# Kernel optimization log

Measured on AMD Instinct MI355X. Metric: run time of the kernel, lower is better.

Reference implementation:

```python
import jax, jax.numpy as jnp
import numpy as np

NMUL = 16
NASH = 3
NEARZERO = 1e-5
TIMESTEP_D = 1.0
LENF = 15

PARAM_BOUNDS = [
    ("schaake_const", 0.0, 0.1), ("smcmax", 0.3, 0.6), ("soil_depth", 0.5, 3.0),
    ("wltsmc", 0.05, 0.2), ("satpsi", 0.01, 0.5), ("bb", 2.0, 12.0),
    ("mult", 100.0, 2000.0), ("satdk", 1e-7, 1e-4), ("slop", 0.0, 1.0),
    ("max_gw_storage", 0.01, 0.5), ("Cgw", 1e-6, 1e-3), ("expon", 1.0, 8.0),
    ("K_nash", 0.01, 0.5),
]
ROUT_BOUNDS = [("rout_a", 0.0, 2.9), ("rout_b", 0.0, 6.5)]


def setup_inputs() -> dict:
    key = jax.random.key(0)
    k1, k2 = jax.random.split(key)
    T, B = 730, 2048
    # prcp ~ U[0,20) mm/d, pet ~ U[0,8) mm/d
    x_phy = jax.random.uniform(k1, (T, B, 2), dtype=jnp.float32) * jnp.array([20.0, 8.0], jnp.float32)
    n_static = len(PARAM_BOUNDS) * NMUL + len(ROUT_BOUNDS)  # 210
    phy_static = jax.random.uniform(k2, (B, n_static), dtype=jnp.float32)
    return {"x_phy": x_phy, "phy_static": phy_static}


def _cfe_forward(x_phy, phy_static):
    T, B, _ = x_phy.shape
    n_phys = len(PARAM_BOUNDS)
    # descale: change_param_range(p, [lb, ub]) = p * (ub - lb) + lb
    phys = phy_static[:, : n_phys * NMUL].reshape(B, n_phys, NMUL)
    prm = {name: phys[:, i, :] * (ub - lb) + lb for i, (name, lb, ub) in enumerate(PARAM_BOUNDS)}
    route_raw = phy_static[:, n_phys * NMUL :]
    rout = {name: route_raw[:, i] * (ub - lb) + lb for i, (name, lb, ub) in enumerate(ROUT_BOUNDS)}

    P = jnp.repeat(x_phy[:, :, 0:1], NMUL, axis=2)    # [T,B,NMUL]
    PET = jnp.repeat(x_phy[:, :, 1:2], NMUL, axis=2)  # [T,B,NMUL]

    soil0 = jnp.full((B, NMUL), 0.05, jnp.float32)
    gw0 = jnp.full((B, NMUL), 0.01, jnp.float32)
    nash0 = jnp.full((B, NMUL, NASH), NEARZERO, jnp.float32)

    max_soil = prm["smcmax"] * prm["soil_depth"]
    # Clapp-Hornberger field-capacity threshold from satpsi, bb
    fc_frac = jnp.clip((prm["satpsi"] / prm["soil_depth"]) ** (1.0 / prm["bb"]), 0.0, 1.0)
    fc_threshold = prm["smcmax"] * fc_frac * prm["soil_depth"]

    def step(carry, forc):
        soil, gw, nash = carry
        p, pet = forc
        # --- ET: first from rainfall, then Budyko-type from soil ---
        et_rain = jnp.minimum(p, pet)
        p_rem = p - et_rain
        pet_rem = pet - et_rain
        smc = soil / prm["soil_depth"]
        budyko = jnp.clip((smc - prm["wltsmc"]) / (prm["smcmax"] - prm["wltsmc"] + NEARZERO), 0.0, 1.0)
        aet_soil = jnp.minimum(pet_rem * budyko, jnp.maximum(soil - NEARZERO, 0.0))
        soil = soil - aet_soil
        aet = et_rain + aet_soil
        # --- Schaake infiltration / runoff partitioning ---
        deficit = jnp.maximum(max_soil - soil, 0.0)
        infil_cap = deficit * (1.0 - jnp.exp(-prm["schaake_const"] * TIMESTEP_D))
        runoff = p_rem * p_rem / (p_rem + infil_cap + NEARZERO)
        runoff = jnp.minimum(runoff, p_rem)
        infiltration = jnp.minimum(p_rem - runoff, deficit)
        runoff = p_rem - infiltration
        soil = soil + infiltration
        # --- soil dual-outlet nonlinear reservoir (percolation + lateral) ---
        above = jnp.maximum(soil - fc_threshold, 0.0)
        frac = above / jnp.maximum(max_soil - fc_threshold, NEARZERO)
        perc = prm["satdk"] * prm["mult"] * TIMESTEP_D * frac
        lat = prm["satdk"] * prm["mult"] * prm["slop"] * TIMESTEP_D * frac
        tot = perc + lat
        scale = jnp.minimum(1.0, above / jnp.maximum(tot, NEARZERO))
        perc = perc * scale
        lat = lat * scale
        soil = soil - perc - lat
        # --- groundwater exponential reservoir ---
        gw = gw + perc
        q_gw = prm["Cgw"] * jnp.expm1(prm["expon"] * jnp.clip(gw / prm["max_gw_storage"], 0.0, 1.0))
        q_gw = jnp.clip(q_gw, 0.0, jnp.maximum(gw - NEARZERO, 0.0))
        gw = gw - q_gw
        # --- Nash cascade routing of lateral flow (3 linear reservoirs) ---
        inflow = lat
        K = prm["K_nash"]
        new_nash = []
        for i in range(NASH):
            s = nash[..., i] + inflow
            out = K * s
            new_nash.append(s - out)
            inflow = out
        nash = jnp.stack(new_nash, axis=-1)
        q_lat = inflow
        q_sim = runoff + q_lat + q_gw
        return (soil, gw, nash), (q_sim, runoff, q_lat, q_gw, aet, soil, gw)

    _, outs = jax.lax.scan(step, (soil0, gw0, nash0), (P, PET))
    q_sim = outs[0]                 # [T,B,NMUL]
    q_avg = q_sim.mean(-1)          # [T,B]  multi-model averaging

    # --- gamma unit-hydrograph routing (uh_gamma + causal uh_conv) ---
    a = jax.nn.relu(rout["rout_a"])[:, None] + 0.1    # [B,1]
    th = jax.nn.relu(rout["rout_b"])[:, None] + 0.5   # [B,1]
    t = (jnp.arange(LENF, dtype=jnp.float32) + 0.5)[None, :]  # [1,LENF]
    w = t ** (a - 1.0) * jnp.exp(-t / th) / (jnp.exp(jax.lax.lgamma(a)) * th ** a)
    w = w / w.sum(1, keepdims=True)                    # [B,LENF]
    xp = jnp.pad(q_avg, ((LENF - 1, 0), (0, 0)))       # causal pad on time axis
    stream = sum(
        w[None, :, j] * jax.lax.dynamic_slice_in_dim(xp, LENF - 1 - j, T, 0)
        for j in range(LENF)
    )
    return stream[..., None]  # [T,B,1] routed streamflow


def reference(x_phy, phy_static):
    return _cfe_forward(x_phy, phy_static)
```

## Files before the change

### kernel.cpp

```cpp
#include <hip/hip_runtime.h>
#include <math.h>


constexpr int T_STEPS = 730;
constexpr int BATCH   = 2048;
constexpr int NMULC   = 16;
constexpr int LENFC   = 15;
constexpr int NPHYS   = 13;
constexpr int NSTAT   = NPHYS * NMULC + 2;
constexpr float NZ    = 1e-5f;
constexpr float INV_NZ= 1e5f;
constexpr int NCH     = 2;
constexpr int LPB     = 8;
constexpr int TB      = 15;
constexpr int T_MAIN  = 720;

__device__ __forceinline__ float frcp(float x) { return __builtin_amdgcn_rcpf(x); }

__device__ __forceinline__ float dpp_sum8(float x) {
    int v;
    v = __builtin_amdgcn_update_dpp(0, __float_as_int(x), 0xB1, 0xF, 0xF, true);
    x += __int_as_float(v);
    v = __builtin_amdgcn_update_dpp(0, __float_as_int(x), 0x4E, 0xF, 0xF, true);
    x += __int_as_float(v);
    v = __builtin_amdgcn_update_dpp(0, __float_as_int(x), 0x141, 0xF, 0xF, true);
    x += __int_as_float(v);
    return x;
}

struct Prm {
    float k1[NCH], k2[NCH], ms[NCH], fc[NCH], ic[NCH], cc[NCH], pc[NCH],
          lc[NCH], sc[NCH], e2[NCH], Km[NCH], Kk[NCH], Cg[NCH], ig[NCH];
    float w[LENFC];
};
struct St { float soil[NCH], gw[NCH], n0[NCH], n1[NCH], n2[NCH]; };

template <int SLOT>
__device__ __forceinline__ float substep(const Prm& P, St& S,
                                         float (&ring)[LENFC], const float2 fv)
{
    const float p = fv.x, pet = fv.y;
    const float et      = fminf(p, pet);
    const float p_rem   = p - et;
    const float pet_rem = pet - et;
    const float prem_nz = p_rem + NZ;
    const float prem_sq = p_rem * p_rem;

    float qsum = 0.0f;
    #pragma unroll
    for (int c = 0; c < NCH; ++c) {
        float budyko = fmaf(S.soil[c], P.k1[c], P.k2[c]);
        budyko = fminf(fmaxf(budyko, 0.0f), 1.0f);
        const float aet = fminf(pet_rem * budyko, S.soil[c] - NZ);
        float so = S.soil[c] - aet;

        const float deficit = P.ms[c] - so;
        const float den     = fmaf(deficit, P.ic[c], prem_nz);
        const float runoff0 = prem_sq * frcp(den);
        const float infil   = fminf(p_rem - runoff0, deficit);
        const float runoff  = p_rem - infil;
        so += infil;

        const float above = fmaxf(so - P.fc[c], 0.0f);
        const float asc   = fminf(above * P.sc[c], above * above * INV_NZ);
        const float lat   = P.lc[c] * asc;
        so = fmaf(-P.cc[c], asc, so);
        S.soil[c] = so;

        float g = fmaf(P.pc[c], asc, S.gw[c]);
        const float ratio = fminf(g * P.ig[c], 1.0f);
        const float qg0   = fmaf(P.Cg[c], __builtin_amdgcn_exp2f(P.e2[c] * ratio), -P.Cg[c]);
        const float qg    = fminf(qg0, g - NZ);
        S.gw[c] = g - qg;

        const float s0 = S.n0[c] + lat;             const float s1 = fmaf(P.Kk[c], s0, S.n1[c]);
        const float s2 = fmaf(P.Kk[c], s1, S.n2[c]); const float o2 = P.Kk[c] * s2;
        S.n0[c] = P.Km[c] * s0; S.n1[c] = P.Km[c] * s1; S.n2[c] = P.Km[c] * s2;

        qsum += runoff + o2 + qg;
    }

    ring[SLOT] = qsum;
    float c0 = 0.0f, c1 = 0.0f, c2 = 0.0f, c3 = 0.0f;
    #pragma unroll
    for (int j = 0; j < LENFC; j += 4) {
        c0 = fmaf(P.w[j], ring[(SLOT - j + 15) % 15], c0);
        if (j + 1 < LENFC) c1 = fmaf(P.w[j + 1], ring[(SLOT - j - 1 + 30) % 15], c1);
        if (j + 2 < LENFC) c2 = fmaf(P.w[j + 2], ring[(SLOT - j - 2 + 30) % 15], c2);
        if (j + 3 < LENFC) c3 = fmaf(P.w[j + 3], ring[(SLOT - j - 3 + 30) % 15], c3);
    }
    return (c0 + c1) + (c2 + c3);
}

#define SUBST(s) { const float acc = substep<(s)>(P, S, ring, f[(s)]);           \
                   const float r = dpp_sum8(acc);                                \
                   if (lane0) out[(tb + (s)) * BATCH + b] = r; }
#define DO15(X) X(0) X(1) X(2) X(3) X(4) X(5) X(6) X(7) X(8) X(9) X(10) X(11) X(12) X(13) X(14)
#define DO10(X) X(0) X(1) X(2) X(3) X(4) X(5) X(6) X(7) X(8) X(9)

__global__ __launch_bounds__(64, 1)
void cfe_kernel(const float* __restrict__ x,
                const float* __restrict__ ps,
                float* __restrict__ out)
{
    const int tid = blockIdx.x * 64 + threadIdx.x;
    const int b   = tid >> 3;
    const int m0  = tid & 7;
    const bool lane0 = (m0 == 0);

    const float* __restrict__ row = ps + b * NSTAT;

    Prm P;
    #pragma unroll
    for (int c = 0; c < NCH; ++c) {
        const int m = m0 + c * 8;
        const float schaake    = row[ 0*NMULC + m] * 0.1f;
        const float smcmax     = row[ 1*NMULC + m] * 0.3f   + 0.3f;
        const float soil_depth = row[ 2*NMULC + m] * 2.5f   + 0.5f;
        const float wltsmc     = row[ 3*NMULC + m] * 0.15f  + 0.05f;
        const float satpsi     = row[ 4*NMULC + m] * 0.49f  + 0.01f;
        const float bb_        = row[ 5*NMULC + m] * 10.0f  + 2.0f;
        const float multp      = row[ 6*NMULC + m] * 1900.0f+ 100.0f;
        const float satdk      = row[ 7*NMULC + m] * (1e-4f - 1e-7f) + 1e-7f;
        const float slop       = row[ 8*NMULC + m];
        const float max_gw     = row[ 9*NMULC + m] * 0.49f  + 0.01f;
        P.Cg[c]                = row[10*NMULC + m] * (1e-3f - 1e-6f) + 1e-6f;
        const float expon      = row[11*NMULC + m] * 7.0f   + 1.0f;
        P.Kk[c]                = row[12*NMULC + m] * 0.49f  + 0.01f;

        const float inv_sd  = 1.0f / soil_depth;
        const float bud_den = 1.0f / (smcmax - wltsmc + NZ);
        P.k1[c] = inv_sd * bud_den;
        P.k2[c] = -wltsmc * bud_den;
        P.ms[c] = smcmax * soil_depth;
        float fc_frac = powf(satpsi * inv_sd, 1.0f / bb_);
        fc_frac = fminf(fmaxf(fc_frac, 0.0f), 1.0f);
        P.fc[c] = smcmax * fc_frac * soil_depth;
        P.ic[c] = 1.0f - expf(-schaake);
        const float sm  = satdk * multp;
        const float sml = sm * slop;
        const float inv_mft = 1.0f / fmaxf(P.ms[c] - P.fc[c], NZ);
        P.ig[c] = 1.0f / max_gw;
        P.cc[c] = inv_mft * (sm + sml);
        P.pc[c] = sm  * inv_mft;
        P.lc[c] = sml * inv_mft;
        P.sc[c] = fminf(1.0f, 1.0f / P.cc[c]);
        P.e2[c] = expon * 1.442695041f;
        P.Km[c] = 1.0f - P.Kk[c];
    }

    {
        const float rout_a = row[NPHYS*NMULC + 0] * 2.9f;
        const float rout_b = row[NPHYS*NMULC + 1] * 6.5f;
        const float a  = fmaxf(rout_a, 0.0f) + 0.1f;
        const float th = fmaxf(rout_b, 0.0f) + 0.5f;
        float wsum = 0.0f;
        #pragma unroll
        for (int j = 0; j < LENFC; ++j) {
            const float tj = (float)j + 0.5f;
            P.w[j] = powf(tj, a - 1.0f) * expf(-tj / th);
            wsum += P.w[j];
        }
        const float wscale = 1.0f / (wsum * (float)NMULC);
        #pragma unroll
        for (int j = 0; j < LENFC; ++j) P.w[j] *= wscale;
    }

    St S;
    #pragma unroll
    for (int c = 0; c < NCH; ++c) {
        S.soil[c] = 0.05f; S.gw[c] = 0.01f;
        S.n0[c] = NZ; S.n1[c] = NZ; S.n2[c] = NZ;
    }
    float ring[LENFC];
    #pragma unroll
    for (int j = 0; j < LENFC; ++j) ring[j] = 0.0f;

    const float2* __restrict__ xp = (const float2*)x;

    #pragma unroll 1
    for (int tb = 0; tb < T_MAIN; tb += TB) {
        float2 f[TB];
        #pragma unroll
        for (int s = 0; s < TB; ++s) f[s] = xp[(tb + s) * BATCH + b];
        DO15(SUBST)
    }

    {
        const int tb = T_MAIN;
        float2 f[10];
        #pragma unroll
        for (int s = 0; s < 10; ++s) f[s] = xp[(tb + s) * BATCH + b];
        DO10(SUBST)
    }
}

extern "C" void kernel_launch(void* const* d_in, const int* in_sizes, int n_in,
                              void* d_out, int out_size, void* d_ws, size_t ws_size,
                              hipStream_t stream) {
    const float* x_phy      = (const float*)d_in[0];
    const float* phy_static = (const float*)d_in[1];
    float* out = (float*)d_out;

    const int total = BATCH * LPB;
    const int block = 64;
    const int grid  = total / block;
    cfe_kernel<<<grid, block, 0, stream>>>(x_phy, phy_static, out);
}
```

Measured before the change: 177.4 us.

## Double-buffer forcing loads and vectorize per-lane physics with float2 ops

Result: faster. 156.0 us (-12.1%).

```diff
diff --git a/kernel.cpp b/kernel.cpp
--- a/kernel.cpp
+++ b/kernel.cpp
@@ -15,7 +15,12 @@
 constexpr int TB      = 15;
 constexpr int T_MAIN  = 720;
 
+typedef float v2f __attribute__((ext_vector_type(2)));
+
 __device__ __forceinline__ float frcp(float x) { return __builtin_amdgcn_rcpf(x); }
+__device__ __forceinline__ v2f v2(float s) { return (v2f){s, s}; }
+__device__ __forceinline__ v2f vmin(v2f a, v2f b) { return __builtin_elementwise_min(a, b); }
+__device__ __forceinline__ v2f vmax(v2f a, v2f b) { return __builtin_elementwise_max(a, b); }
 
 __device__ __forceinline__ float dpp_sum8(float x) {
     int v;
@@ -29,11 +34,10 @@
 }
 
 struct Prm {
-    float k1[NCH], k2[NCH], ms[NCH], fc[NCH], ic[NCH], cc[NCH], pc[NCH],
-          lc[NCH], sc[NCH], e2[NCH], Km[NCH], Kk[NCH], Cg[NCH], ig[NCH];
+    v2f k1, k2, ms, fc, ic, cc, pc, lc, sc, e2, Km, Kk, Cg, ig;
     float w[LENFC];
 };
-struct St { float soil[NCH], gw[NCH], n0[NCH], n1[NCH], n2[NCH]; };
+struct St { v2f soil, gw, n0, n1, n2; };
 
 template <int SLOT>
 __device__ __forceinline__ float substep(const Prm& P, St& S,
@@ -46,39 +50,42 @@
     const float prem_nz = p_rem + NZ;
     const float prem_sq = p_rem * p_rem;
 
-    float qsum = 0.0f;
-    #pragma unroll
-    for (int c = 0; c < NCH; ++c) {
-        float budyko = fmaf(S.soil[c], P.k1[c], P.k2[c]);
-        budyko = fminf(fmaxf(budyko, 0.0f), 1.0f);
-        const float aet = fminf(pet_rem * budyko, S.soil[c] - NZ);
-        float so = S.soil[c] - aet;
-
-        const float deficit = P.ms[c] - so;
-        const float den     = fmaf(deficit, P.ic[c], prem_nz);
-        const float runoff0 = prem_sq * frcp(den);
-        const float infil   = fminf(p_rem - runoff0, deficit);
-        const float runoff  = p_rem - infil;
-        so += infil;
-
-        const float above = fmaxf(so - P.fc[c], 0.0f);
-        const float asc   = fminf(above * P.sc[c], above * above * INV_NZ);
-        const float lat   = P.lc[c] * asc;
-        so = fmaf(-P.cc[c], asc, so);
-        S.soil[c] = so;
-
-        float g = fmaf(P.pc[c], asc, S.gw[c]);
-        const float ratio = fminf(g * P.ig[c], 1.0f);
-        const float qg0   = fmaf(P.Cg[c], __builtin_amdgcn_exp2f(P.e2[c] * ratio), -P.Cg[c]);
-        const float qg    = fminf(qg0, g - NZ);
-        S.gw[c] = g - qg;
-
-        const float s0 = S.n0[c] + lat;             const float s1 = fmaf(P.Kk[c], s0, S.n1[c]);
-        const float s2 = fmaf(P.Kk[c], s1, S.n2[c]); const float o2 = P.Kk[c] * s2;
-        S.n0[c] = P.Km[c] * s0; S.n1[c] = P.Km[c] * s1; S.n2[c] = P.Km[c] * s2;
-
-        qsum += runoff + o2 + qg;
-    }
+    v2f budyko = S.soil * P.k1 + P.k2;
+    budyko = vmin(vmax(budyko, v2(0.0f)), v2(1.0f));
+    const v2f aet = vmin(v2(pet_rem) * budyko, S.soil - v2(NZ));
+    v2f so = S.soil - aet;
+
+    const v2f deficit = P.ms - so;
+    const v2f den     = deficit * P.ic + v2(prem_nz);
+    v2f rden; rden.x = frcp(den.x); rden.y = frcp(den.y);
+    const v2f runoff0 = v2(prem_sq) * rden;
+    const v2f infil   = vmin(v2(p_rem) - runoff0, deficit);
+    const v2f runoff  = v2(p_rem) - infil;
+    so += infil;
+
+    const v2f above = vmax(so - P.fc, v2(0.0f));
+    const v2f asc   = vmin(above * P.sc, above * above * v2(INV_NZ));
+    const v2f lat   = P.lc * asc;
+    so = so - P.cc * asc;
+    S.soil = so;
+
+    v2f g = P.pc * asc + S.gw;
+    const v2f ratio = vmin(g * P.ig, v2(1.0f));
+    v2f ex;
+    ex.x = __builtin_amdgcn_exp2f(P.e2.x * ratio.x);
+    ex.y = __builtin_amdgcn_exp2f(P.e2.y * ratio.y);
+    const v2f qg0 = P.Cg * ex - P.Cg;
+    const v2f qg  = vmin(qg0, g - v2(NZ));
+    S.gw = g - qg;
+
+    const v2f s0 = S.n0 + lat;
+    const v2f s1 = P.Kk * s0 + S.n1;
+    const v2f s2 = P.Kk * s1 + S.n2;
+    const v2f o2 = P.Kk * s2;
+    S.n0 = P.Km * s0; S.n1 = P.Km * s1; S.n2 = P.Km * s2;
+
+    const v2f qv = runoff + o2 + qg;
+    const float qsum = qv.x + qv.y;
 
     ring[SLOT] = qsum;
     float c0 = 0.0f, c1 = 0.0f, c2 = 0.0f, c3 = 0.0f;
@@ -92,11 +99,21 @@
     return (c0 + c1) + (c2 + c3);
 }
 
-#define SUBST(s) { const float acc = substep<(s)>(P, S, ring, f[(s)]);           \
-                   const float r = dpp_sum8(acc);                                \
-                   if (lane0) out[(tb + (s)) * BATCH + b] = r; }
-#define DO15(X) X(0) X(1) X(2) X(3) X(4) X(5) X(6) X(7) X(8) X(9) X(10) X(11) X(12) X(13) X(14)
-#define DO10(X) X(0) X(1) X(2) X(3) X(4) X(5) X(6) X(7) X(8) X(9)
+#define SUBST(s, FBUF, TBASE) {                                              \
+    const float acc = substep<(s)>(P, S, ring, FBUF[(s)]);                   \
+    const float r = dpp_sum8(acc);                                           \
+    if (lane0) out[((TBASE) + (s)) * BATCH + b] = r; }
+#define DO15(FBUF, TBASE) \
+    SUBST(0,FBUF,TBASE) SUBST(1,FBUF,TBASE) SUBST(2,FBUF,TBASE)  \
+    SUBST(3,FBUF,TBASE) SUBST(4,FBUF,TBASE) SUBST(5,FBUF,TBASE)  \
+    SUBST(6,FBUF,TBASE) SUBST(7,FBUF,TBASE) SUBST(8,FBUF,TBASE)  \
+    SUBST(9,FBUF,TBASE) SUBST(10,FBUF,TBASE) SUBST(11,FBUF,TBASE)\
+    SUBST(12,FBUF,TBASE) SUBST(13,FBUF,TBASE) SUBST(14,FBUF,TBASE)
+#define DO10(FBUF, TBASE) \
+    SUBST(0,FBUF,TBASE) SUBST(1,FBUF,TBASE) SUBST(2,FBUF,TBASE)  \
+    SUBST(3,FBUF,TBASE) SUBST(4,FBUF,TBASE) SUBST(5,FBUF,TBASE)  \
+    SUBST(6,FBUF,TBASE) SUBST(7,FBUF,TBASE) SUBST(8,FBUF,TBASE)  \
+    SUBST(9,FBUF,TBASE)
 
 __global__ __launch_bounds__(64, 1)
 void cfe_kernel(const float* __restrict__ x,
@@ -124,29 +141,35 @@
         const float satdk      = row[ 7*NMULC + m] * (1e-4f - 1e-7f) + 1e-7f;
         const float slop       = row[ 8*NMULC + m];
         const float max_gw     = row[ 9*NMULC + m] * 0.49f  + 0.01f;
-        P.Cg[c]                = row[10*NMULC + m] * (1e-3f - 1e-6f) + 1e-6f;
+        const float Cgw        = row[10*NMULC + m] * (1e-3f - 1e-6f) + 1e-6f;
         const float expon      = row[11*NMULC + m] * 7.0f   + 1.0f;
-        P.Kk[c]                = row[12*NMULC + m] * 0.49f  + 0.01f;
+        const float K          = row[12*NMULC + m] * 0.49f  + 0.01f;
 
         const float inv_sd  = 1.0f / soil_depth;
         const float bud_den = 1.0f / (smcmax - wltsmc + NZ);
+        const float ms      = smcmax * soil_depth;
+        float fc_frac = powf(satpsi * inv_sd, 1.0f / bb_);
+        fc_frac = fminf(fmaxf(fc_frac, 0.0f), 1.0f);
+        const float fc      = smcmax * fc_frac * soil_depth;
+        const float sm      = satdk * multp;
+        const float sml     = sm * slop;
+        const float inv_mft = 1.0f / fmaxf(ms - fc, NZ);
+        const float ccv     = inv_mft * (sm + sml);
+
         P.k1[c] = inv_sd * bud_den;
         P.k2[c] = -wltsmc * bud_den;
-        P.ms[c] = smcmax * soil_depth;
-        float fc_frac = powf(satpsi * inv_sd, 1.0f / bb_);
-        fc_frac = fminf(fmaxf(fc_frac, 0.0f), 1.0f);
-        P.fc[c] = smcmax * fc_frac * soil_depth;
+        P.ms[c] = ms;
+        P.fc[c] = fc;
         P.ic[c] = 1.0f - expf(-schaake);
-        const float sm  = satdk * multp;
-        const float sml = sm * slop;
-        const float inv_mft = 1.0f / fmaxf(P.ms[c] - P.fc[c], NZ);
-        P.ig[c] = 1.0f / max_gw;
-        P.cc[c] = inv_mft * (sm + sml);
+        P.cc[c] = ccv;
         P.pc[c] = sm  * inv_mft;
         P.lc[c] = sml * inv_mft;
-        P.sc[c] = fminf(1.0f, 1.0f / P.cc[c]);
+        P.sc[c] = fminf(1.0f, 1.0f / ccv);
         P.e2[c] = expon * 1.442695041f;
-        P.Km[c] = 1.0f - P.Kk[c];
+        P.Km[c] = 1.0f - K;
+        P.Kk[c] = K;
+        P.Cg[c] = Cgw;
+        P.ig[c] = 1.0f / max_gw;
     }
 
     {
@@ -167,32 +190,35 @@
     }
 
     St S;
-    #pragma unroll
-    for (int c = 0; c < NCH; ++c) {
-        S.soil[c] = 0.05f; S.gw[c] = 0.01f;
-        S.n0[c] = NZ; S.n1[c] = NZ; S.n2[c] = NZ;
-    }
+    S.soil = v2(0.05f); S.gw = v2(0.01f);
+    S.n0 = v2(NZ); S.n1 = v2(NZ); S.n2 = v2(NZ);
     float ring[LENFC];
     #pragma unroll
     for (int j = 0; j < LENFC; ++j) ring[j] = 0.0f;
 
     const float2* __restrict__ xp = (const float2*)x;
 
+    float2 fA[TB], fB[TB];
+    #pragma unroll
+    for (int s = 0; s < TB; ++s) fA[s] = xp[s * BATCH + b];
+
     #pragma unroll 1
-    for (int tb = 0; tb < T_MAIN; tb += TB) {
-        float2 f[TB];
-        #pragma unroll
-        for (int s = 0; s < TB; ++s) f[s] = xp[(tb + s) * BATCH + b];
-        DO15(SUBST)
-    }
-
-    {
-        const int tb = T_MAIN;
-        float2 f[10];
-        #pragma unroll
-        for (int s = 0; s < 10; ++s) f[s] = xp[(tb + s) * BATCH + b];
-        DO10(SUBST)
-    }
+    for (int tb = 0; tb < T_MAIN; tb += 2 * TB) {
+        #pragma unroll
+        for (int s = 0; s < TB; ++s) {
+            int t = tb + TB + s; if (t > T_STEPS - 1) t = T_STEPS - 1;
+            fB[s] = xp[t * BATCH + b];
+        }
+        DO15(fA, tb)
+        #pragma unroll
+        for (int s = 0; s < TB; ++s) {
+            int t = tb + 2 * TB + s; if (t > T_STEPS - 1) t = T_STEPS - 1;
+            fA[s] = xp[t * BATCH + b];
+        }
+        DO15(fB, tb + TB)
+    }
+
+    DO10(fA, T_MAIN)
 }
 
 extern "C" void kernel_launch(void* const* d_in, const int* in_sizes, int n_in,
```
